# Optimization experiments

Hardware: AMD Instinct MI355X
Metric: run time of the kernel (lower is better)

Reference implementation:

```python
import jax, jax.numpy as jnp
import numpy as np

D_IN = 16
D_OUT = 8
HIDDEN = 64


def setup_inputs() -> dict:
    key = jax.random.key(0)
    ks = jax.random.split(key, 8)
    B = 524288
    x = jax.random.normal(ks[0], (B, D_IN), dtype=jnp.float32)
    # scalar attention weights for the two attention blocks, shape [2, 1]
    wq = jax.random.normal(ks[1], (2, 1), dtype=jnp.float32)
    wk = jax.random.normal(ks[2], (2, 1), dtype=jnp.float32)
    wv = jax.random.normal(ks[3], (2, 1), dtype=jnp.float32)
    # hidden: Linear(16 -> HIDDEN), output: Linear(HIDDEN -> 8)
    lim_h = 1.0 / np.sqrt(D_IN)
    Wh = jax.random.uniform(ks[4], (HIDDEN, D_IN), minval=-lim_h, maxval=lim_h, dtype=jnp.float32)
    bh = jax.random.uniform(ks[5], (HIDDEN,), minval=-lim_h, maxval=lim_h, dtype=jnp.float32)
    lim_o = 1.0 / np.sqrt(HIDDEN)
    Wo = jax.random.uniform(ks[6], (D_OUT, HIDDEN), minval=-lim_o, maxval=lim_o, dtype=jnp.float32)
    bo = jax.random.uniform(ks[7], (D_OUT,), minval=-lim_o, maxval=lim_o, dtype=jnp.float32)
    return {"x": x, "wq": wq, "wk": wk, "wv": wv, "Wh": Wh, "bh": bh, "Wo": Wo, "bo": bo}


def _self_attention(x, q, k, v):
    # x: [B, D]; q, k, v: scalars. Q=K=V are scalar-scaled copies of x.
    Q = q * x  # [B, D]
    K = k * x
    V = v * x
    # Alpha[b, i, j] = K[b, i] * Q[b, j]  (outer product, matches Kt @ Q)
    Alpha = K[:, :, None] * Q[:, None, :]  # [B, D, D]
    A = jax.nn.softmax(Alpha, axis=2)
    # O[b, j] = sum_i V[b, i] * A[b, i, j]  (matches V @ AlphaD)
    return jnp.einsum('bi,bij->bj', V, A)  # [B, D]


def reference(x, wq, wk, wv, Wh, bh, Wo, bo):
    o1 = _self_attention(x[:, 0:16], wq[0, 0], wk[0, 0], wv[0, 0])  # [B, 16]
    x1 = jax.nn.sigmoid(o1 @ Wh.T + bh)                              # [B, HIDDEN]
    x2 = x1 @ Wo.T + bo                                              # [B, 8]
    o2 = _self_attention(x2, wq[1, 0], wk[1, 0], wv[1, 0])          # [B, 8]
    w = jax.nn.softmax(o2, axis=1)                                   # [B, 8]
    # out = x[:, None, 8:16] @ w[:, :, None]  -> [B, 1, 1]
    out = jnp.einsum('bi,bi->b', x[:, 8:16], w)[:, None, None]
    return out
```

## Files before the change

kernel.cpp:

```cpp
#include <hip/hip_runtime.h>


__device__ __forceinline__ float rcpf(float a) { return __builtin_amdgcn_rcpf(a); }

__global__ __launch_bounds__(256) void fused_attn_mlp(
    const float* __restrict__ x,
    const float* __restrict__ wq,
    const float* __restrict__ wk,
    const float* __restrict__ wv,
    const float* __restrict__ Wh,
    const float* __restrict__ bh,
    const float* __restrict__ Wo,
    const float* __restrict__ bo,
    float* __restrict__ out,
    int B)
{
    const int b = blockIdx.x * blockDim.x + threadIdx.x;
    if (b >= B) return;

    float xv[16];
    const float4* xr = reinterpret_cast<const float4*>(x) + (size_t)b * 4;
    float4 a0 = xr[0], a1 = xr[1], a2 = xr[2], a3 = xr[3];
    xv[0] = a0.x; xv[1] = a0.y; xv[2]  = a0.z; xv[3]  = a0.w;
    xv[4] = a1.x; xv[5] = a1.y; xv[6]  = a1.z; xv[7]  = a1.w;
    xv[8] = a2.x; xv[9] = a2.y; xv[10] = a2.z; xv[11] = a2.w;
    xv[12] = a3.x; xv[13] = a3.y; xv[14] = a3.z; xv[15] = a3.w;

    const float kq1 = wk[0] * wq[0];
    const float v1  = wv[0];

    float xmx = xv[0], xmn = xv[0];
    #pragma unroll
    for (int i = 1; i < 16; ++i) { xmx = fmaxf(xmx, xv[i]); xmn = fminf(xmn, xv[i]); }

    float o1[16];
    #pragma unroll
    for (int j = 0; j < 16; ++j) o1[j] = 0.f;

    #pragma unroll
    for (int i = 0; i < 16; ++i) {
        const float c = kq1 * xv[i];
        const float m = fmaxf(c * xmx, c * xmn);
        float e[16], s = 0.f;
        #pragma unroll
        for (int j = 0; j < 16; ++j) { e[j] = __expf(c * xv[j] - m); s += e[j]; }
        const float w = v1 * xv[i] * rcpf(s);
        #pragma unroll
        for (int j = 0; j < 16; ++j) o1[j] += w * e[j];
    }

    float x2[8];
    #pragma unroll
    for (int o = 0; o < 8; ++o) x2[o] = bo[o];

    #pragma unroll 8
    for (int h = 0; h < 64; ++h) {
        float acc = bh[h];
        #pragma unroll
        for (int i = 0; i < 16; ++i) acc += o1[i] * Wh[h * 16 + i];
        const float sg = rcpf(1.f + __expf(-acc));
        #pragma unroll
        for (int o = 0; o < 8; ++o) x2[o] += Wo[o * 64 + h] * sg;
    }

    const float kq2 = wk[1] * wq[1];
    const float v2  = wv[1];

    float ymx = x2[0], ymn = x2[0];
    #pragma unroll
    for (int i = 1; i < 8; ++i) { ymx = fmaxf(ymx, x2[i]); ymn = fminf(ymn, x2[i]); }

    float o2[8];
    #pragma unroll
    for (int j = 0; j < 8; ++j) o2[j] = 0.f;

    #pragma unroll
    for (int i = 0; i < 8; ++i) {
        const float c = kq2 * x2[i];
        const float m = fmaxf(c * ymx, c * ymn);
        float e[8], s = 0.f;
        #pragma unroll
        for (int j = 0; j < 8; ++j) { e[j] = __expf(c * x2[j] - m); s += e[j]; }
        const float w = v2 * x2[i] * rcpf(s);
        #pragma unroll
        for (int j = 0; j < 8; ++j) o2[j] += w * e[j];
    }

    float m2 = o2[0];
    #pragma unroll
    for (int i = 1; i < 8; ++i) m2 = fmaxf(m2, o2[i]);
    float s2 = 0.f, dot = 0.f;
    #pragma unroll
    for (int i = 0; i < 8; ++i) {
        const float e = __expf(o2[i] - m2);
        s2 += e;
        dot += xv[8 + i] * e;
    }
    out[b] = dot * rcpf(s2);
}

extern "C" void kernel_launch(void* const* d_in, const int* in_sizes, int n_in,
                              void* d_out, int out_size, void* d_ws, size_t ws_size,
                              hipStream_t stream) {
    const float* x  = (const float*)d_in[0];
    const float* wq = (const float*)d_in[1];
    const float* wk = (const float*)d_in[2];
    const float* wv = (const float*)d_in[3];
    const float* Wh = (const float*)d_in[4];
    const float* bh = (const float*)d_in[5];
    const float* Wo = (const float*)d_in[6];
    const float* bo = (const float*)d_in[7];
    float* out = (float*)d_out;

    const int B = in_sizes[0] / 16;
    const int block = 256;
    const int grid = (B + block - 1) / block;
    fused_attn_mlp<<<grid, block, 0, stream>>>(x, wq, wk, wv, Wh, bh, Wo, bo, out, B);
}
```

Before: 144.2 us.

## Use packed float2 math, exp2 with folded log2e, and LDS-staged MLP weights

The kernel folds log2(e) into the attention scale constants so each exponential becomes a single native exp2 instruction without an extra multiply. Elementwise math is rewritten on two-wide float vectors so the compiler can emit packed FMA/mul instructions. The MLP weights Wh, a transposed Wo and bh are staged into shared memory at block start, so the hidden-layer loop reads LDS instead of issuing repeated scalar global loads. This adds a block-level barrier and LDS traffic, and the packed ops only help if the compiler actually forms them.

```diff
diff --git a/kernel.cpp b/kernel.cpp
--- a/kernel.cpp
+++ b/kernel.cpp
@@ -1,7 +1,17 @@
 #include <hip/hip_runtime.h>
 
 
+typedef float v2f __attribute__((ext_vector_type(2)));
+
+#define LOG2E 1.44269504088896340736f
+
 __device__ __forceinline__ float rcpf(float a) { return __builtin_amdgcn_rcpf(a); }
+
+#if __has_builtin(__builtin_amdgcn_exp2f)
+__device__ __forceinline__ float exp2_fast(float a) { return __builtin_amdgcn_exp2f(a); }
+#else
+__device__ __forceinline__ float exp2_fast(float a) { return __expf(0.6931471805599453f * a); }
+#endif
 
 __global__ __launch_bounds__(256) void fused_attn_mlp(
     const float* __restrict__ x,
@@ -15,86 +25,137 @@
     float* __restrict__ out,
     int B)
 {
-    const int b = blockIdx.x * blockDim.x + threadIdx.x;
+    __shared__ float sWh[64 * 16];
+    __shared__ float sWoT[64 * 8];
+    __shared__ float sbh[64];
+
+    const int t = threadIdx.x;
+    {
+        const float4* src = reinterpret_cast<const float4*>(Wh);
+        float4* dst = reinterpret_cast<float4*>(sWh);
+        dst[t] = src[t];
+    }
+    #pragma unroll
+    for (int r = t; r < 512; r += 256) {
+        const int h = r >> 3, o = r & 7;
+        sWoT[h * 8 + o] = Wo[o * 64 + h];
+    }
+    if (t < 64) sbh[t] = bh[t];
+    __syncthreads();
+
+    const int b = blockIdx.x * blockDim.x + t;
     if (b >= B) return;
 
-    float xv[16];
-    const float4* xr = reinterpret_cast<const float4*>(x) + (size_t)b * 4;
-    float4 a0 = xr[0], a1 = xr[1], a2 = xr[2], a3 = xr[3];
-    xv[0] = a0.x; xv[1] = a0.y; xv[2]  = a0.z; xv[3]  = a0.w;
-    xv[4] = a1.x; xv[5] = a1.y; xv[6]  = a1.z; xv[7]  = a1.w;
-    xv[8] = a2.x; xv[9] = a2.y; xv[10] = a2.z; xv[11] = a2.w;
-    xv[12] = a3.x; xv[13] = a3.y; xv[14] = a3.z; xv[15] = a3.w;
+    float xs[16];
+    {
+        const float4* xr = reinterpret_cast<const float4*>(x) + (size_t)b * 4;
+        float4 a0 = xr[0], a1 = xr[1], a2 = xr[2], a3 = xr[3];
+        xs[0]=a0.x; xs[1]=a0.y; xs[2]=a0.z; xs[3]=a0.w;
+        xs[4]=a1.x; xs[5]=a1.y; xs[6]=a1.z; xs[7]=a1.w;
+        xs[8]=a2.x; xs[9]=a2.y; xs[10]=a2.z; xs[11]=a2.w;
+        xs[12]=a3.x; xs[13]=a3.y; xs[14]=a3.z; xs[15]=a3.w;
+    }
+    v2f xv2[8];
+    #pragma unroll
+    for (int p = 0; p < 8; ++p) { v2f v; v[0] = xs[2*p]; v[1] = xs[2*p+1]; xv2[p] = v; }
 
-    const float kq1 = wk[0] * wq[0];
+    const float kq1 = wk[0] * wq[0] * LOG2E;
     const float v1  = wv[0];
 
-    float xmx = xv[0], xmn = xv[0];
+    float xmx = xs[0], xmn = xs[0];
     #pragma unroll
-    for (int i = 1; i < 16; ++i) { xmx = fmaxf(xmx, xv[i]); xmn = fminf(xmn, xv[i]); }
+    for (int i = 1; i < 16; ++i) { xmx = fmaxf(xmx, xs[i]); xmn = fminf(xmn, xs[i]); }
 
-    float o1[16];
+    v2f o1v[8];
     #pragma unroll
-    for (int j = 0; j < 16; ++j) o1[j] = 0.f;
+    for (int p = 0; p < 8; ++p) o1v[p] = (v2f)(0.f);
 
     #pragma unroll
     for (int i = 0; i < 16; ++i) {
-        const float c = kq1 * xv[i];
+        const float c = kq1 * xs[i];
         const float m = fmaxf(c * xmx, c * xmn);
-        float e[16], s = 0.f;
+        v2f cc; cc[0] = c; cc[1] = c;
+        v2f mm; mm[0] = m; mm[1] = m;
+        v2f e2[8], sv = (v2f)(0.f);
         #pragma unroll
-        for (int j = 0; j < 16; ++j) { e[j] = __expf(c * xv[j] - m); s += e[j]; }
-        const float w = v1 * xv[i] * rcpf(s);
+        for (int p = 0; p < 8; ++p) {
+            v2f a = cc * xv2[p] - mm;
+            v2f e; e[0] = exp2_fast(a[0]); e[1] = exp2_fast(a[1]);
+            e2[p] = e;
+            sv += e;
+        }
+        const float s = sv[0] + sv[1];
+        const float w = v1 * xs[i] * rcpf(s);
+        v2f ww; ww[0] = w; ww[1] = w;
         #pragma unroll
-        for (int j = 0; j < 16; ++j) o1[j] += w * e[j];
+        for (int p = 0; p < 8; ++p) o1v[p] += ww * e2[p];
     }
 
-    float x2[8];
+    v2f x2v[4];
     #pragma unroll
-    for (int o = 0; o < 8; ++o) x2[o] = bo[o];
+    for (int p = 0; p < 4; ++p) { v2f v; v[0] = bo[2*p]; v[1] = bo[2*p+1]; x2v[p] = v; }
 
     #pragma unroll 8
     for (int h = 0; h < 64; ++h) {
-        float acc = bh[h];
+        const v2f* wh = reinterpret_cast<const v2f*>(sWh + h * 16);
+        v2f acc = wh[0] * o1v[0];
         #pragma unroll
-        for (int i = 0; i < 16; ++i) acc += o1[i] * Wh[h * 16 + i];
-        const float sg = rcpf(1.f + __expf(-acc));
+        for (int p = 1; p < 8; ++p) acc += wh[p] * o1v[p];
+        const float a = acc[0] + acc[1] + sbh[h];
+        const float sg = rcpf(1.f + exp2_fast(-a * LOG2E));
+        const v2f* wo = reinterpret_cast<const v2f*>(sWoT + h * 8);
+        v2f sgv; sgv[0] = sg; sgv[1] = sg;
         #pragma unroll
-        for (int o = 0; o < 8; ++o) x2[o] += Wo[o * 64 + h] * sg;
+        for (int p = 0; p < 4; ++p) x2v[p] += wo[p] * sgv;
     }
 
-    const float kq2 = wk[1] * wq[1];
-    const float v2  = wv[1];
+    const float kq2 = wk[1] * wq[1] * LOG2E;
+    const float v2s = wv[1] * LOG2E;
 
-    float ymx = x2[0], ymn = x2[0];
+    float ys[8];
     #pragma unroll
-    for (int i = 1; i < 8; ++i) { ymx = fmaxf(ymx, x2[i]); ymn = fminf(ymn, x2[i]); }
+    for (int i = 0; i < 8; ++i) ys[i] = x2v[i >> 1][i & 1];
+    float ymx = ys[0], ymn = ys[0];
+    #pragma unroll
+    for (int i = 1; i < 8; ++i) { ymx = fmaxf(ymx, ys[i]); ymn = fminf(ymn, ys[i]); }
 
-    float o2[8];
+    v2f o2v[4];
     #pragma unroll
-    for (int j = 0; j < 8; ++j) o2[j] = 0.f;
+    for (int p = 0; p < 4; ++p) o2v[p] = (v2f)(0.f);
 
     #pragma unroll
     for (int i = 0; i < 8; ++i) {
-        const float c = kq2 * x2[i];
+        const float c = kq2 * ys[i];
         const float m = fmaxf(c * ymx, c * ymn);
-        float e[8], s = 0.f;
+        v2f cc; cc[0] = c; cc[1] = c;
+        v2f mm; mm[0] = m; mm[1] = m;
+        v2f e2[4], sv = (v2f)(0.f);
         #pragma unroll
-        for (int j = 0; j < 8; ++j) { e[j] = __expf(c * x2[j] - m); s += e[j]; }
-        const float w = v2 * x2[i] * rcpf(s);
+        for (int p = 0; p < 4; ++p) {
+            v2f a = cc * x2v[p] - mm;
+            v2f e; e[0] = exp2_fast(a[0]); e[1] = exp2_fast(a[1]);
+            e2[p] = e;
+            sv += e;
+        }
+        const float s = sv[0] + sv[1];
+        const float w = v2s * ys[i] * rcpf(s);
+        v2f ww; ww[0] = w; ww[1] = w;
         #pragma unroll
-        for (int j = 0; j < 8; ++j) o2[j] += w * e[j];
+        for (int p = 0; p < 4; ++p) o2v[p] += ww * e2[p];
     }
 
-    float m2 = o2[0];
+    float o2s[8];
     #pragma unroll
-    for (int i = 1; i < 8; ++i) m2 = fmaxf(m2, o2[i]);
+    for (int i = 0; i < 8; ++i) o2s[i] = o2v[i >> 1][i & 1];
+    float m2 = o2s[0];
+    #pragma unroll
+    for (int i = 1; i < 8; ++i) m2 = fmaxf(m2, o2s[i]);
     float s2 = 0.f, dot = 0.f;
     #pragma unroll
     for (int i = 0; i < 8; ++i) {
-        const float e = __expf(o2[i] - m2);
+        const float e = exp2_fast(o2s[i] - m2);
         s2 += e;
-        dot += xv[8 + i] * e;
+        dot += xs[8 + i] * e;
     }
     out[b] = dot * rcpf(s2);
 }
```

New measurement: 132.3 us. 1.09x faster.
